# Kernel tuning notes

Hardware: AMD Instinct MI355X
Metric: run time of the kernel (lower is better)

The kernel has to match this reference:

```python
import jax, jax.numpy as jnp
import numpy as np
from jax import lax

B, SQ, SK, D, K = 4, 2048, 2048, 1024, 3


def setup_inputs() -> dict:
    key = jax.random.key(0)
    ks = jax.random.split(key, 16)
    s = 0.02
    return {
        "query_hidden": jax.random.normal(ks[0], (B, SQ, D), jnp.float32),
        "memory_hidden": jax.random.normal(ks[1], (B, SK, D), jnp.float32),
        "attention_mask": jax.random.randint(ks[2], (SQ, SK), 0, 2).astype(bool),
        # Linear projections (torch: y = x @ W.T + b)
        "q_w": jax.random.normal(ks[3], (D, D), jnp.float32) * s,
        "q_b": jnp.zeros((D,), jnp.float32),
        "k_w": jax.random.normal(ks[4], (D, D), jnp.float32) * s,
        "k_b": jnp.zeros((D,), jnp.float32),
        "v_w": jax.random.normal(ks[5], (D, D), jnp.float32) * s,
        "v_b": jnp.zeros((D,), jnp.float32),
        "o_w": jax.random.normal(ks[6], (D, D), jnp.float32) * s,
        "o_b": jnp.zeros((D,), jnp.float32),
        # ConvTransform1D: depthwise conv kernels [D,1,K], bias [D], scalar gate
        "q_kernel": jax.random.normal(ks[7], (D, 1, K), jnp.float32) * s,
        "q_cbias": jnp.zeros((D,), jnp.float32),
        "q_gate": jnp.zeros((), jnp.float32),
        "k_kernel": jax.random.normal(ks[8], (D, 1, K), jnp.float32) * s,
        "k_cbias": jnp.zeros((D,), jnp.float32),
        "k_gate": jnp.zeros((), jnp.float32),
        "v_kernel": jax.random.normal(ks[9], (D, 1, K), jnp.float32) * s,
        "v_cbias": jnp.zeros((D,), jnp.float32),
        "v_gate": jnp.zeros((), jnp.float32),
    }


def _conv_transform(x, kernel, cbias, gate):
    """Gated depthwise 1D conv along seq: x + tanh(gate) * dwconv(x). x: [B,S,D]."""
    xc = jnp.transpose(x, (0, 2, 1))  # [B,D,S]
    y = lax.conv_general_dilated(
        xc, kernel, window_strides=(1,), padding="SAME",
        dimension_numbers=("NCH", "OIH", "NCH"), feature_group_count=x.shape[-1])
    y = y + cbias[None, :, None]
    return x + jnp.tanh(gate) * jnp.transpose(y, (0, 2, 1))


def reference(query_hidden, memory_hidden, attention_mask,
              q_w, q_b, k_w, k_b, v_w, v_b, o_w, o_b,
              q_kernel, q_cbias, q_gate,
              k_kernel, k_cbias, k_gate,
              v_kernel, v_cbias, v_gate):
    d_model = query_hidden.shape[-1]
    q = _conv_transform(query_hidden @ q_w.T + q_b, q_kernel, q_cbias, q_gate)
    k = _conv_transform(memory_hidden @ k_w.T + k_b, k_kernel, k_cbias, k_gate)
    v = _conv_transform(memory_hidden @ v_w.T + v_b, v_kernel, v_cbias, v_gate)
    # [B,Sq,Sk]
    logits = jnp.einsum("bqd,bkd->bqk", q, k) / jnp.sqrt(jnp.float32(d_model))
    mask = attention_mask[None, :, :]  # broadcast like torch unsqueeze(0)
    logits = jnp.where(mask, logits, jnp.finfo(logits.dtype).min)
    attn = jax.nn.softmax(logits, axis=-1)
    out = jnp.einsum("bqk,bkd->bqd", attn, v) @ o_w.T + o_b
    return out
```

## Files before the change

### kernel.cpp

```cpp
#include <hip/hip_runtime.h>
#include <cstdint>
#include <cstddef>


#define GLOBAL_AS __attribute__((address_space(1)))
#define LDS_AS    __attribute__((address_space(3)))

typedef _Float16 h8 __attribute__((ext_vector_type(8)));
typedef float    f4_t __attribute__((ext_vector_type(4)));
typedef unsigned short us8 __attribute__((ext_vector_type(8)));

__device__ __forceinline__ float bf2f(unsigned short u) {
    union { unsigned int i; float f; } x; x.i = ((unsigned int)u) << 16; return x.f;
}
__device__ __forceinline__ float rd(const void* p, long i, int isBf) {
    return isBf ? bf2f(((const unsigned short*)p)[i]) : ((const float*)p)[i];
}

struct Probe16 { const unsigned short* p[16]; int n[16]; };

__global__ void k_probes(Probe16 a, const unsigned int* __restrict__ mask,
                         int* __restrict__ flags) {
    if (blockIdx.x < 16) {
        __shared__ int cnt;
        if (threadIdx.x == 0) cnt = 0;
        __syncthreads();
        const unsigned short* s = a.p[blockIdx.x];
        const int n = a.n[blockIdx.x];
        int bad = 0;
        for (int i = threadIdx.x; i < n; i += 256) {
            int e = (s[i] >> 7) & 0xFF;
            if (e >= 0x8F || (e > 0 && e <= 0x60)) bad++;
        }
        atomicAdd(&cnt, bad);
        __syncthreads();
        if (threadIdx.x == 0) flags[blockIdx.x] = (cnt * 4 > n) ? 0 : 1;
    } else {
        __shared__ int vi32, vf32, vbf, vf16;
        if (threadIdx.x == 0) { vi32 = vf32 = vbf = vf16 = 0; }
        __syncthreads();
        int bi32 = 0, bf32 = 0, bbf = 0, bf16c = 0;
        for (int i = threadIdx.x; i < 4096; i += 256) {
            unsigned int w = mask[i];
            if (!(w == 0u || w == 1u)) bi32++;
            if (!(w == 0u || w == 0x3F800000u)) bf32++;
            unsigned int h0 = w & 0xFFFFu, h1 = w >> 16;
            if (!((h0 == 0u || h0 == 0x3F80u) && (h1 == 0u || h1 == 0x3F80u))) bbf++;
            if (!((h0 == 0u || h0 == 0x3C00u) && (h1 == 0u || h1 == 0x3C00u))) bf16c++;
        }
        if (bi32) atomicAdd(&vi32, 1);
        if (bf32) atomicAdd(&vf32, 1);
        if (bbf)  atomicAdd(&vbf, 1);
        if (bf16c) atomicAdd(&vf16, 1);
        __syncthreads();
        if (threadIdx.x == 0) {
            int w;
            if (vi32 == 0) w = 4;
            else if (vf32 == 0) w = 4;
            else if (vbf == 0) w = 2;
            else if (vf16 == 0) w = 2;
            else w = 1;
            flags[16] = w;
        }
    }
}

__global__ void k_mask_bytes(const void* __restrict__ m, unsigned char* __restrict__ out,
                             long n, const int* __restrict__ widthFlag) {
    long i = ((long)blockIdx.x * 256 + threadIdx.x) * 4;
    if (i >= n) return;
    const int w = *widthFlag;
    unsigned int packed = 0;
    if (w == 4) {
        const unsigned int* p = (const unsigned int*)m;
#pragma unroll
        for (int u = 0; u < 4; ++u) packed |= (p[i + u] != 0u ? 1u : 0u) << (8 * u);
    } else if (w == 2) {
        const unsigned short* p = (const unsigned short*)m;
#pragma unroll
        for (int u = 0; u < 4; ++u) packed |= (p[i + u] != 0u ? 1u : 0u) << (8 * u);
    } else {
        const unsigned char* p = (const unsigned char*)m;
#pragma unroll
        for (int u = 0; u < 4; ++u) packed |= (p[i + u] != 0u ? 1u : 0u) << (8 * u);
    }
    *(unsigned int*)(out + i) = packed;
}

struct ConvSrc { const void* kern[3]; const void* cb[3]; const void* gate[3]; };
__global__ void k_conv_params(ConvSrc p, const int* __restrict__ flags,
                              _Float16* __restrict__ out, float* __restrict__ tg, int D) {
#pragma unroll
    for (int t = 0; t < 3; ++t) {
        const int kIs = flags[6 + t], cIs = flags[13 + t];
        for (int d = threadIdx.x; d < D; d += 256) {
#pragma unroll
            for (int j = 0; j < 3; ++j)
                out[t * 3 * D + j * D + d] = (_Float16)rd(p.kern[t], (long)d * 3 + j, kIs);
            out[9 * D + t * D + d] = (_Float16)rd(p.cb[t], d, cIs);
        }
    }
    if (threadIdx.x < 3) {
        const void* g = p.gate[threadIdx.x];
        float gv = rd(g, 0, ((const unsigned int*)g)[0] == 0u ? 1 : 0);
        tg[threadIdx.x] = tanhf(gv);
    }
}

__device__ __forceinline__ h8 cvt8(const void* src, size_t off8, int isBf) {
    h8 d;
    if (isBf) {
        us8 s = *(const us8*)((const unsigned short*)src + off8 * 8);
#pragma unroll
        for (int u = 0; u < 8; ++u) d[u] = (_Float16)bf2f(s[u]);
    } else {
        const float* f = (const float*)src + off8 * 8;
        f4_t a = *(const f4_t*)f;
        f4_t b = *(const f4_t*)(f + 4);
#pragma unroll
        for (int u = 0; u < 4; ++u) { d[u] = (_Float16)a[u]; d[4 + u] = (_Float16)b[u]; }
    }
    return d;
}

__global__ void k_h_to_f16(const void* __restrict__ s0, const void* __restrict__ s1,
                           _Float16* __restrict__ dst, int n8each,
                           const int* __restrict__ flags) {
    int i = blockIdx.x * blockDim.x + threadIdx.x;
    if (i >= 2 * n8each) return;
    int seg = i / n8each, off = i - seg * n8each;
    h8 d = cvt8(seg ? s1 : s0, off, flags[seg]);
    *(h8*)(dst + (size_t)i * 8) = d;
}

struct Ptr4 { const void* p[4]; };
__global__ void k_w_to_f16(Ptr4 srcs, _Float16* __restrict__ dst, int n8each,
                           const int* __restrict__ flags) {
    int i = blockIdx.x * blockDim.x + threadIdx.x;
    if (i >= 4 * n8each) return;
    int seg = i / n8each, off = i - seg * n8each;
    h8 d = cvt8(srcs.p[seg], off, flags[seg]);
    *(h8*)(dst + (size_t)i * 8) = d;
}

template <int MODE, int MTILE>
__global__ __launch_bounds__(256, 4) void k_gemm_nt(
    const _Float16* __restrict__ A, const _Float16* __restrict__ Bm,
    void* __restrict__ Cout,
    const void* __restrict__ bias, const int* __restrict__ biasFlag,
    const void* __restrict__ bias2, const int* __restrict__ biasFlag2,
    int N, int K, long sA, long sB, long sC,
    float scale, const unsigned char* __restrict__ mask8,
    int NT, int BZ) {

    constexpr int NI = (MTILE == 128) ? 4 : 2;
    constexpr int NCA = MTILE / 32;
    __shared__ __align__(16) _Float16 As[MTILE * 64];
    __shared__ __align__(16) _Float16 Bs[128 * 64];

    const long id = blockIdx.x;
    const int xcd = (int)(id & 7);
    const long local = id >> 3;
    const int col = (int)(local % NT);
    const long g = (local / NT) * 8 + xcd;
    const int bz = (int)(g % BZ);
    const int brow = (int)(g / BZ);

    const int tid  = threadIdx.x;
    const int wave = tid >> 6, lane = tid & 63;
    const int wm = (wave >> 1) * (MTILE / 2), wn = (wave & 1) * 64;
    const int lr = lane & 15, lq = lane >> 4;

    const _Float16* Ab = A + (long)bz * sA + (size_t)brow * MTILE * K;
    const _Float16* Bb = Bm + (long)bz * sB + (size_t)col * 128 * K;

    f4_t acc[NI][4] = {};

    const _Float16* gA[NCA];
    _Float16* lA[NCA];
#pragma unroll
    for (int j = 0; j < NCA; ++j) {
        int c = tid + j * 256;
        int r = c >> 3, s = ((c & 7) - r) & 7;
        gA[j] = Ab + (size_t)r * K + s * 8;
        lA[j] = As + c * 8;
    }
    const _Float16* gB[4];
    _Float16* lB[4];
#pragma unroll
    for (int j = 0; j < 4; ++j) {
        int c = tid + j * 256;
        int r = c >> 3, s = ((c & 7) - r) & 7;
        gB[j] = Bb + (size_t)r * K + s * 8;
        lB[j] = Bs + c * 8;
    }

    for (int kb = 0; kb < K; kb += 64) {
#pragma unroll
        for (int j = 0; j < NCA; ++j)
            __builtin_amdgcn_global_load_lds((void GLOBAL_AS*)(gA[j] + kb), (void LDS_AS*)lA[j], 16, 0, 0);
#pragma unroll
        for (int j = 0; j < 4; ++j)
            __builtin_amdgcn_global_load_lds((void GLOBAL_AS*)(gB[j] + kb), (void LDS_AS*)lB[j], 16, 0, 0);
        __syncthreads();

#pragma unroll
        for (int t = 0; t < 2; ++t) {
            const int fs = ((t * 4 + lq + lr) & 7) * 8;
            h8 af[NI], bfr[4];
#pragma unroll
            for (int i = 0; i < NI; ++i) af[i]  = *(const h8*)&As[(wm + i * 16 + lr) * 64 + fs];
#pragma unroll
            for (int j = 0; j < 4; ++j) bfr[j] = *(const h8*)&Bs[(wn + j * 16 + lr) * 64 + fs];
#pragma unroll
            for (int i = 0; i < NI; ++i)
#pragma unroll
                for (int j = 0; j < 4; ++j)
                    acc[i][j] = __builtin_amdgcn_mfma_f32_16x16x32_f16(af[i], bfr[j], acc[i][j], 0, 0, 0);
        }
        __syncthreads();
    }

    const long row0 = (long)brow * MTILE + wm + lq * 4;
    const long col0 = (long)col * 128 + wn + lr;

    if constexpr (MODE == 3) {
        _Float16* C = (_Float16*)Cout + (long)bz * sC;
#pragma unroll
        for (int i = 0; i < NI; ++i)
#pragma unroll
            for (int j = 0; j < 4; ++j)
#pragma unroll
                for (int r = 0; r < 4; ++r) {
                    long row = row0 + i * 16 + r;
                    long ccol = col0 + j * 16;
                    bool keep = mask8[row * (long)N + ccol] != 0;
                    float v = acc[i][j][r] * scale;
                    v = fminf(fmaxf(v, -60000.0f), 60000.0f);
                    C[row * (long)N + ccol] = (_Float16)(keep ? v : -60000.0f);
                }
    } else {
        float bv[4];
        if constexpr (MODE != 0) {
            const void* bp = bias; const int* bfp = biasFlag; long boff = 0;
            if (bias2 != nullptr && col * 128 >= (N >> 1)) {
                bp = bias2; bfp = biasFlag2; boff = (long)(N >> 1);
            }
            const int bIs = *bfp;
#pragma unroll
            for (int j = 0; j < 4; ++j) bv[j] = rd(bp, col0 + j * 16 - boff, bIs);
        } else {
#pragma unroll
            for (int j = 0; j < 4; ++j) bv[j] = 0.0f;
        }
        if constexpr (MODE == 2) {
            float* C = (float*)Cout + (long)bz * sC;
#pragma unroll
            for (int i = 0; i < NI; ++i)
#pragma unroll
                for (int j = 0; j < 4; ++j)
#pragma unroll
                    for (int r = 0; r < 4; ++r)
                        C[(row0 + i * 16 + r) * (long)N + col0 + j * 16] = acc[i][j][r] + bv[j];
        } else {
            _Float16* C = (_Float16*)Cout + (long)bz * sC;
#pragma unroll
            for (int i = 0; i < NI; ++i)
#pragma unroll
                for (int j = 0; j < 4; ++j)
#pragma unroll
                    for (int r = 0; r < 4; ++r) {
                        float v = acc[i][j][r] + bv[j];
                        v = fminf(fmaxf(v, -65000.0f), 65000.0f);
                        C[(row0 + i * 16 + r) * (long)N + col0 + j * 16] = (_Float16)v;
                    }
        }
    }
}

struct ConvP {
    const _Float16* x; int xs; _Float16* y;
    const _Float16* kp; const _Float16* cb; const float* tg;
};
__global__ void k_dwconv2(ConvP p0, ConvP p1, int S, int D) {
    const ConvP& p = blockIdx.z ? p1 : p0;
    int s = blockIdx.x, b = blockIdx.y;
    int d0 = threadIdx.x * 8;
    const size_t xb = ((size_t)b * S + s) * p.xs + d0;
    const size_t yb = ((size_t)b * S + s) * D + d0;
    h8 zero;
#pragma unroll
    for (int u = 0; u < 8; ++u) zero[u] = (_Float16)0.0f;
    h8 xc = *(const h8*)(p.x + xb);
    h8 xp = (s > 0)     ? *(const h8*)(p.x + xb - p.xs) : zero;
    h8 xn = (s < S - 1) ? *(const h8*)(p.x + xb + p.xs) : zero;
    h8 k0 = *(const h8*)(p.kp + 0 * D + d0);
    h8 k1 = *(const h8*)(p.kp + 1 * D + d0);
    h8 k2 = *(const h8*)(p.kp + 2 * D + d0);
    h8 cb = *(const h8*)(p.cb + d0);
    float tg = *p.tg;
    h8 o;
#pragma unroll
    for (int u = 0; u < 8; ++u) {
        float cv = (float)xp[u] * (float)k0[u] + (float)xc[u] * (float)k1[u] +
                   (float)xn[u] * (float)k2[u] + (float)cb[u];
        float v = (float)xc[u] + tg * cv;
        o[u] = (_Float16)fminf(fmaxf(v, -65000.0f), 65000.0f);
    }
    *(h8*)(p.y + yb) = o;
}

__global__ void k_dwconv_t(const _Float16* __restrict__ x, int xs,
                           _Float16* __restrict__ vt,
                           const _Float16* __restrict__ kp,
                           const _Float16* __restrict__ cbp,
                           const float* __restrict__ tgp,
                           int SK, int D) {
    __shared__ _Float16 T[64][65];
    int b = blockIdx.z;
    int s0 = blockIdx.x * 64, d0 = blockIdx.y * 64;
    int tid = threadIdx.x;
    float tg = *tgp;
    h8 zero;
#pragma unroll
    for (int u = 0; u < 8; ++u) zero[u] = (_Float16)0.0f;
#pragma unroll
    for (int it = 0; it < 2; ++it) {
        int idx = it * 256 + tid;
        int r = idx >> 3, c = (idx & 7) * 8;
        int s = s0 + r;
        const size_t xb = ((size_t)b * SK + s) * xs + d0 + c;
        h8 xc = *(const h8*)(x + xb);
        h8 xp = (s > 0)      ? *(const h8*)(x + xb - xs) : zero;
        h8 xn = (s < SK - 1) ? *(const h8*)(x + xb + xs) : zero;
        h8 k0 = *(const h8*)(kp + 0 * D + d0 + c);
        h8 k1 = *(const h8*)(kp + 1 * D + d0 + c);
        h8 k2 = *(const h8*)(kp + 2 * D + d0 + c);
        h8 cb = *(const h8*)(cbp + d0 + c);
#pragma unroll
        for (int u = 0; u < 8; ++u) {
            float cv = (float)xp[u] * (float)k0[u] + (float)xc[u] * (float)k1[u] +
                       (float)xn[u] * (float)k2[u] + (float)cb[u];
            float v = (float)xc[u] + tg * cv;
            T[r][c + u] = (_Float16)fminf(fmaxf(v, -65000.0f), 65000.0f);
        }
    }
    __syncthreads();
#pragma unroll
    for (int it = 0; it < 2; ++it) {
        int idx = it * 256 + tid;
        int dr = idx >> 3, c = (idx & 7) * 8;
        h8 o;
#pragma unroll
        for (int u = 0; u < 8; ++u) o[u] = T[c + u][dr];
        *(h8*)(vt + ((size_t)b * D + d0 + dr) * SK + s0 + c) = o;
    }
}

__global__ __launch_bounds__(256) void k_softmax(const _Float16* __restrict__ sc,
                                                 _Float16* __restrict__ pr, int SK) {
    const long row = blockIdx.x;
    const int tid = threadIdx.x, lane = tid & 63, wave = tid >> 6;
    h8 v = *(const h8*)(sc + row * (long)SK + tid * 8);
    float f[8]; float mx = -3.0e38f;
#pragma unroll
    for (int u = 0; u < 8; ++u) { f[u] = (float)v[u]; mx = fmaxf(mx, f[u]); }
#pragma unroll
    for (int o = 32; o > 0; o >>= 1) mx = fmaxf(mx, __shfl_xor(mx, o, 64));
    __shared__ float red[8];
    if (lane == 0) red[wave] = mx;
    __syncthreads();
    mx = fmaxf(fmaxf(red[0], red[1]), fmaxf(red[2], red[3]));
    float sum = 0.0f;
#pragma unroll
    for (int u = 0; u < 8; ++u) { f[u] = __expf(f[u] - mx); sum += f[u]; }
#pragma unroll
    for (int o = 32; o > 0; o >>= 1) sum += __shfl_xor(sum, o, 64);
    if (lane == 0) red[4 + wave] = sum;
    __syncthreads();
    sum = red[4] + red[5] + red[6] + red[7];
    float inv = 1.0f / sum;
    h8 o8;
#pragma unroll
    for (int u = 0; u < 8; ++u) o8[u] = (_Float16)(f[u] * inv);
    *(h8*)(pr + row * (long)SK + tid * 8) = o8;
}

extern "C" void kernel_launch(void* const* d_in, const int* in_sizes, int n_in,
                              void* d_out, int out_size, void* d_ws, size_t ws_size,
                              hipStream_t stream) {
    const int Bn = 4, SQ = 2048, SK = 2048, D = 1024;
    const size_t nQ = (size_t)Bn * SQ * D;
    const long   nM = (long)SQ * SK;

    const void* qh = d_in[0];
    const void* mh = d_in[1];
    const void* mask = d_in[2];
    const void* q_w = d_in[3];
    const void* q_b = d_in[4];
    const void* k_w = d_in[5];
    const void* k_b = d_in[6];
    const void* v_w = d_in[7];
    const void* v_b = d_in[8];
    const void* o_w = d_in[9];
    const void* o_b = d_in[10];
    const void* q_kern = d_in[11];
    const void* q_cb   = d_in[12];
    const void* q_g    = d_in[13];
    const void* k_kern = d_in[14];
    const void* k_cb   = d_in[15];
    const void* k_g    = d_in[16];
    const void* v_kern = d_in[17];
    const void* v_cb   = d_in[18];
    const void* v_g    = d_in[19];

    char* ws = (char*)d_ws;
    _Float16* scores   = (_Float16*)(ws + 0);
    _Float16* attn_out = (_Float16*)(ws + 0);
    _Float16* w16      = (_Float16*)(ws + 33554432);
    unsigned char* mask8 = (unsigned char*)(ws + 33554432);
    _Float16* par16    = (_Float16*)(ws + 37748736);
    float*    tgf      = (float*)(ws + 37748736 + 12 * 1024 * 2);
    _Float16* lin      = (_Float16*)(ws + 41943040);
    _Float16* lin_q    = lin;
    _Float16* lin_kv   = lin + nQ;
    _Float16* probs    = lin;
    _Float16* conv     = (_Float16*)(ws + 92274688);
    _Float16* qh16     = conv;
    _Float16* mh16     = conv + nQ;
    _Float16* vt       = (_Float16*)(ws + 125829120);
    int*      flags    = (int*)(ws + 142606336);

    Probe16 pa;
    const void* pp[16] = {qh, mh, q_w, k_w, v_w, o_w, q_kern, k_kern, v_kern,
                          q_b, k_b, v_b, o_b, q_cb, k_cb, v_cb};
    const int   pn[16] = {2048, 2048, 2048, 2048, 2048, 2048, 3072, 3072, 3072,
                          1024, 1024, 1024, 1024, 1024, 1024, 1024};
    for (int i = 0; i < 16; ++i) { pa.p[i] = (const unsigned short*)pp[i]; pa.n[i] = pn[i]; }
    k_probes<<<17, 256, 0, stream>>>(pa, (const unsigned int*)mask, flags);

    const int nH8 = (int)(nQ / 8);
    k_h_to_f16<<<(2 * nH8 + 255) / 256, 256, 0, stream>>>(qh, mh, qh16, nH8, flags + 0);
    const int nW8 = D * D / 8;
    Ptr4 wp; wp.p[0] = q_w; wp.p[1] = k_w; wp.p[2] = v_w; wp.p[3] = o_w;
    k_w_to_f16<<<(4 * nW8 + 255) / 256, 256, 0, stream>>>(wp, w16, nW8, flags + 2);

    k_gemm_nt<1, 64><<<dim3(1024), 256, 0, stream>>>(
        qh16, w16, lin_q, q_b, flags + 9, nullptr, nullptr,
        D, D, 0, 0, 0, 1.0f, nullptr, 8, 1);
    k_gemm_nt<1, 128><<<dim3(1024), 256, 0, stream>>>(
        mh16, w16 + (size_t)D * D, lin_kv, k_b, flags + 10, v_b, flags + 11,
        2 * D, D, 0, 0, 0, 1.0f, nullptr, 16, 1);

    k_mask_bytes<<<(int)(nM / 4 / 256), 256, 0, stream>>>(mask, mask8, nM, flags + 16);
    ConvSrc cs;
    cs.kern[0] = q_kern; cs.kern[1] = k_kern; cs.kern[2] = v_kern;
    cs.cb[0] = q_cb; cs.cb[1] = k_cb; cs.cb[2] = v_cb;
    cs.gate[0] = q_g; cs.gate[1] = k_g; cs.gate[2] = v_g;
    k_conv_params<<<1, 256, 0, stream>>>(cs, flags, par16, tgf, D);

    ConvP cq{lin_q, D, conv + 0 * nQ, par16 + 0 * 3 * D, par16 + 9 * D + 0 * D, tgf + 0};
    ConvP ck{lin_kv, 2 * D, conv + 1 * nQ, par16 + 1 * 3 * D, par16 + 9 * D + 1 * D, tgf + 1};
    k_dwconv2<<<dim3(SQ, Bn, 2), 128, 0, stream>>>(cq, ck, SQ, D);
    k_dwconv_t<<<dim3(SK / 64, D / 64, Bn), 256, 0, stream>>>(
        lin_kv + D, 2 * D, vt, par16 + 2 * 3 * D, par16 + 9 * D + 2 * D, tgf + 2, SK, D);

    k_gemm_nt<3, 128><<<dim3(1024), 256, 0, stream>>>(
        conv + 0 * nQ, conv + 1 * nQ, scores, nullptr, nullptr, nullptr, nullptr,
        SK, D, (long)SQ * D, (long)SK * D, (long)SQ * SK, 0.03125f, mask8, 16, 4);

    k_softmax<<<Bn * SQ, 256, 0, stream>>>(scores, probs, SK);

    k_gemm_nt<0, 64><<<dim3(1024), 256, 0, stream>>>(
        probs, vt, attn_out, nullptr, nullptr, nullptr, nullptr,
        D, SK, (long)SQ * SK, (long)D * SK, (long)SQ * D, 1.0f, nullptr, 8, 4);

    k_gemm_nt<2, 64><<<dim3(1024), 256, 0, stream>>>(
        attn_out, w16 + 3 * (size_t)D * D, d_out, o_b, flags + 12, nullptr, nullptr,
        D, D, 0, 0, 0, 1.0f, nullptr, 8, 1);

    (void)in_sizes; (void)n_in; (void)out_size; (void)ws_size;
}
```

Baseline: 409.4 us.

## Replace GEMMs with 8-wave 256x128 double-buffered pipelined kernel

Replaces the 4-wave, single-buffered NT GEMM with a 512-thread kernel that computes a 256x128 tile per block. It double-buffers A and B in LDS, issuing the next k-tile's global-to-LDS loads in two halves interleaved with the MFMA phases, and uses explicit vmcnt waits, barriers and setprio. The aim is to hide global load latency behind compute and raise per-block data reuse. The cost is 96KB of LDS per block, fewer blocks (256-512 instead of 1024), and correctness that depends on hand-placed waitcnt and barrier ordering.

Result: no change. 410.9 us (+0.4%).

```diff
diff --git a/kernel.cpp b/kernel.cpp
--- a/kernel.cpp
+++ b/kernel.cpp
@@ -143,8 +143,8 @@
     *(h8*)(dst + (size_t)i * 8) = d;
 }
 
-template <int MODE, int MTILE>
-__global__ __launch_bounds__(256, 4) void k_gemm_nt(
+template <int MODE>
+__global__ __launch_bounds__(512, 2) void k_gemm8(
     const _Float16* __restrict__ A, const _Float16* __restrict__ Bm,
     void* __restrict__ Cout,
     const void* __restrict__ bias, const int* __restrict__ biasFlag,
@@ -153,10 +153,8 @@
     float scale, const unsigned char* __restrict__ mask8,
     int NT, int BZ) {
 
-    constexpr int NI = (MTILE == 128) ? 4 : 2;
-    constexpr int NCA = MTILE / 32;
-    __shared__ __align__(16) _Float16 As[MTILE * 64];
-    __shared__ __align__(16) _Float16 Bs[128 * 64];
+    __shared__ __align__(16) _Float16 AS[2][256 * 64];
+    __shared__ __align__(16) _Float16 BS[2][128 * 64];
 
     const long id = blockIdx.x;
     const int xcd = (int)(id & 7);
@@ -168,66 +166,121 @@
 
     const int tid  = threadIdx.x;
     const int wave = tid >> 6, lane = tid & 63;
-    const int wm = (wave >> 1) * (MTILE / 2), wn = (wave & 1) * 64;
+    const int wr = wave >> 1, wc = wave & 1;
+    const int wmRow = wr * 64, wnRow = wc * 64;
     const int lr = lane & 15, lq = lane >> 4;
 
-    const _Float16* Ab = A + (long)bz * sA + (size_t)brow * MTILE * K;
+    const _Float16* Ab = A + (long)bz * sA + (size_t)brow * 256 * K;
     const _Float16* Bb = Bm + (long)bz * sB + (size_t)col * 128 * K;
 
-    f4_t acc[NI][4] = {};
-
-    const _Float16* gA[NCA];
-    _Float16* lA[NCA];
-#pragma unroll
-    for (int j = 0; j < NCA; ++j) {
-        int c = tid + j * 256;
+    f4_t acc[4][4] = {};
+
+    const _Float16* gA[4]; int lA[4];
+#pragma unroll
+    for (int j = 0; j < 4; ++j) {
+        int c = (tid & 255) + (j + 4 * (tid >> 8)) * 256;
         int r = c >> 3, s = ((c & 7) - r) & 7;
         gA[j] = Ab + (size_t)r * K + s * 8;
-        lA[j] = As + c * 8;
-    }
-    const _Float16* gB[4];
-    _Float16* lB[4];
-#pragma unroll
-    for (int j = 0; j < 4; ++j) {
-        int c = tid + j * 256;
+        lA[j] = c * 8;
+    }
+    const _Float16* gB[2]; int lB[2];
+#pragma unroll
+    for (int j = 0; j < 2; ++j) {
+        int c = tid + j * 512;
         int r = c >> 3, s = ((c & 7) - r) & 7;
         gB[j] = Bb + (size_t)r * K + s * 8;
-        lB[j] = Bs + c * 8;
-    }
-
-    for (int kb = 0; kb < K; kb += 64) {
-#pragma unroll
-        for (int j = 0; j < NCA; ++j)
-            __builtin_amdgcn_global_load_lds((void GLOBAL_AS*)(gA[j] + kb), (void LDS_AS*)lA[j], 16, 0, 0);
-#pragma unroll
-        for (int j = 0; j < 4; ++j)
-            __builtin_amdgcn_global_load_lds((void GLOBAL_AS*)(gB[j] + kb), (void LDS_AS*)lB[j], 16, 0, 0);
-        __syncthreads();
-
-#pragma unroll
-        for (int t = 0; t < 2; ++t) {
-            const int fs = ((t * 4 + lq + lr) & 7) * 8;
-            h8 af[NI], bfr[4];
-#pragma unroll
-            for (int i = 0; i < NI; ++i) af[i]  = *(const h8*)&As[(wm + i * 16 + lr) * 64 + fs];
-#pragma unroll
-            for (int j = 0; j < 4; ++j) bfr[j] = *(const h8*)&Bs[(wn + j * 16 + lr) * 64 + fs];
-#pragma unroll
-            for (int i = 0; i < NI; ++i)
-#pragma unroll
-                for (int j = 0; j < 4; ++j)
-                    acc[i][j] = __builtin_amdgcn_mfma_f32_16x16x32_f16(af[i], bfr[j], acc[i][j], 0, 0, 0);
-        }
-        __syncthreads();
-    }
-
-    const long row0 = (long)brow * MTILE + wm + lq * 4;
-    const long col0 = (long)col * 128 + wn + lr;
+        lB[j] = c * 8;
+    }
+
+    const int nkt = K >> 6;
+
+    __builtin_amdgcn_global_load_lds((void GLOBAL_AS*)gB[0], (void LDS_AS*)&BS[0][lB[0]], 16, 0, 0);
+    __builtin_amdgcn_global_load_lds((void GLOBAL_AS*)gB[1], (void LDS_AS*)&BS[0][lB[1]], 16, 0, 0);
+    __builtin_amdgcn_global_load_lds((void GLOBAL_AS*)gA[0], (void LDS_AS*)&AS[0][lA[0]], 16, 0, 0);
+    __builtin_amdgcn_global_load_lds((void GLOBAL_AS*)gA[2], (void LDS_AS*)&AS[0][lA[2]], 16, 0, 0);
+    __builtin_amdgcn_global_load_lds((void GLOBAL_AS*)gA[1], (void LDS_AS*)&AS[0][lA[1]], 16, 0, 0);
+    __builtin_amdgcn_global_load_lds((void GLOBAL_AS*)gA[3], (void LDS_AS*)&AS[0][lA[3]], 16, 0, 0);
+    asm volatile("s_waitcnt vmcnt(2)" ::: "memory");
+    __builtin_amdgcn_s_barrier();
+
+    int p = 0;
+    for (int t = 0; t < nkt; ++t) {
+        const _Float16* Ac = &AS[p][0];
+        const _Float16* Bc = &BS[p][0];
+        _Float16* An = &AS[p ^ 1][0];
+        _Float16* Bn = &BS[p ^ 1][0];
+        const bool pf = (t + 1) < nkt;
+        const long kb = (long)(t + 1) << 6;
+
+        h8 bfr[4][2], a0[2][2];
+#pragma unroll
+        for (int ks = 0; ks < 2; ++ks) {
+            const int fs = ((ks * 4 + lq + lr) & 7) * 8;
+#pragma unroll
+            for (int n = 0; n < 4; ++n)
+                bfr[n][ks] = *(const h8*)&Bc[(wnRow + n * 16 + lr) * 64 + fs];
+#pragma unroll
+            for (int i = 0; i < 2; ++i)
+                a0[i][ks] = *(const h8*)&Ac[(wmRow + i * 16 + lr) * 64 + fs];
+        }
+        if (pf) {
+            __builtin_amdgcn_global_load_lds((void GLOBAL_AS*)(gB[0] + kb), (void LDS_AS*)&Bn[lB[0]], 16, 0, 0);
+            __builtin_amdgcn_global_load_lds((void GLOBAL_AS*)(gB[1] + kb), (void LDS_AS*)&Bn[lB[1]], 16, 0, 0);
+            __builtin_amdgcn_global_load_lds((void GLOBAL_AS*)(gA[0] + kb), (void LDS_AS*)&An[lA[0]], 16, 0, 0);
+            __builtin_amdgcn_global_load_lds((void GLOBAL_AS*)(gA[2] + kb), (void LDS_AS*)&An[lA[2]], 16, 0, 0);
+        }
+        __builtin_amdgcn_s_barrier();
+        __builtin_amdgcn_s_setprio(1);
+#pragma unroll
+        for (int ks = 0; ks < 2; ++ks)
+#pragma unroll
+            for (int i = 0; i < 2; ++i)
+#pragma unroll
+                for (int n = 0; n < 4; ++n)
+                    acc[i][n] = __builtin_amdgcn_mfma_f32_16x16x32_f16(
+                        a0[i][ks], bfr[n][ks], acc[i][n], 0, 0, 0);
+        __builtin_amdgcn_s_setprio(0);
+        if (pf) asm volatile("s_waitcnt vmcnt(4)" ::: "memory");
+        else    asm volatile("s_waitcnt vmcnt(0)" ::: "memory");
+        __builtin_amdgcn_s_barrier();
+
+        h8 a1[2][2];
+#pragma unroll
+        for (int ks = 0; ks < 2; ++ks) {
+            const int fs = ((ks * 4 + lq + lr) & 7) * 8;
+#pragma unroll
+            for (int i = 0; i < 2; ++i)
+                a1[i][ks] = *(const h8*)&Ac[(wmRow + 32 + i * 16 + lr) * 64 + fs];
+        }
+        if (pf) {
+            __builtin_amdgcn_global_load_lds((void GLOBAL_AS*)(gA[1] + kb), (void LDS_AS*)&An[lA[1]], 16, 0, 0);
+            __builtin_amdgcn_global_load_lds((void GLOBAL_AS*)(gA[3] + kb), (void LDS_AS*)&An[lA[3]], 16, 0, 0);
+        }
+        __builtin_amdgcn_s_barrier();
+        __builtin_amdgcn_s_setprio(1);
+#pragma unroll
+        for (int ks = 0; ks < 2; ++ks)
+#pragma unroll
+            for (int i = 0; i < 2; ++i)
+#pragma unroll
+                for (int n = 0; n < 4; ++n)
+                    acc[2 + i][n] = __builtin_amdgcn_mfma_f32_16x16x32_f16(
+                        a1[i][ks], bfr[n][ks], acc[2 + i][n], 0, 0, 0);
+        __builtin_amdgcn_s_setprio(0);
+        if (pf) {
+            asm volatile("s_waitcnt vmcnt(2)" ::: "memory");
+            __builtin_amdgcn_s_barrier();
+        }
+        p ^= 1;
+    }
+
+    const long row0 = (long)brow * 256 + wmRow + lq * 4;
+    const long col0 = (long)col * 128 + wnRow + lr;
 
     if constexpr (MODE == 3) {
         _Float16* C = (_Float16*)Cout + (long)bz * sC;
 #pragma unroll
-        for (int i = 0; i < NI; ++i)
+        for (int i = 0; i < 4; ++i)
 #pragma unroll
             for (int j = 0; j < 4; ++j)
 #pragma unroll
@@ -256,7 +309,7 @@
         if constexpr (MODE == 2) {
             float* C = (float*)Cout + (long)bz * sC;
 #pragma unroll
-            for (int i = 0; i < NI; ++i)
+            for (int i = 0; i < 4; ++i)
 #pragma unroll
                 for (int j = 0; j < 4; ++j)
 #pragma unroll
@@ -265,7 +318,7 @@
         } else {
             _Float16* C = (_Float16*)Cout + (long)bz * sC;
 #pragma unroll
-            for (int i = 0; i < NI; ++i)
+            for (int i = 0; i < 4; ++i)
 #pragma unroll
                 for (int j = 0; j < 4; ++j)
 #pragma unroll
@@ -445,10 +498,10 @@
     Ptr4 wp; wp.p[0] = q_w; wp.p[1] = k_w; wp.p[2] = v_w; wp.p[3] = o_w;
     k_w_to_f16<<<(4 * nW8 + 255) / 256, 256, 0, stream>>>(wp, w16, nW8, flags + 2);
 
-    k_gemm_nt<1, 64><<<dim3(1024), 256, 0, stream>>>(
+    k_gemm8<1><<<dim3(256), 512, 0, stream>>>(
         qh16, w16, lin_q, q_b, flags + 9, nullptr, nullptr,
         D, D, 0, 0, 0, 1.0f, nullptr, 8, 1);
-    k_gemm_nt<1, 128><<<dim3(1024), 256, 0, stream>>>(
+    k_gemm8<1><<<dim3(512), 512, 0, stream>>>(
         mh16, w16 + (size_t)D * D, lin_kv, k_b, flags + 10, v_b, flags + 11,
         2 * D, D, 0, 0, 0, 1.0f, nullptr, 16, 1);
 
@@ -465,17 +518,17 @@
     k_dwconv_t<<<dim3(SK / 64, D / 64, Bn), 256, 0, stream>>>(
         lin_kv + D, 2 * D, vt, par16 + 2 * 3 * D, par16 + 9 * D + 2 * D, tgf + 2, SK, D);
 
-    k_gemm_nt<3, 128><<<dim3(1024), 256, 0, stream>>>(
+    k_gemm8<3><<<dim3(512), 512, 0, stream>>>(
         conv + 0 * nQ, conv + 1 * nQ, scores, nullptr, nullptr, nullptr, nullptr,
         SK, D, (long)SQ * D, (long)SK * D, (long)SQ * SK, 0.03125f, mask8, 16, 4);
 
     k_softmax<<<Bn * SQ, 256, 0, stream>>>(scores, probs, SK);
 
-    k_gemm_nt<0, 64><<<dim3(1024), 256, 0, stream>>>(
+    k_gemm8<0><<<dim3(256), 512, 0, stream>>>(
         probs, vt, attn_out, nullptr, nullptr, nullptr, nullptr,
         D, SK, (long)SQ * SK, (long)D * SK, (long)SQ * D, 1.0f, nullptr, 8, 4);
 
-    k_gemm_nt<2, 64><<<dim3(1024), 256, 0, stream>>>(
+    k_gemm8<2><<<dim3(256), 512, 0, stream>>>(
         attn_out, w16 + 3 * (size_t)D * D, d_out, o_b, flags + 12, nullptr, nullptr,
         D, D, 0, 0, 0, 1.0f, nullptr, 8, 1);
 
```

## Add 256x256-tile 8-wave GEMM with LDS-direct loads for KV and QK^T

Applied to the files above, without the earlier changes.

Adds a new k_gemm16 kernel with 256x256 output tiles, 512 threads (8 waves), double-buffered LDS fed by global_load_lds, and a four-phase interleaved schedule that prefetches quarter-tiles while running MFMAs at raised priority. The KV projection and the masked QK^T score GEMM now use it instead of the 128-wide k_gemm_nt. The aim is more data reuse per tile and better overlap of loads with compute. In exchange it uses large LDS and many registers, and only 256 blocks are launched. The old k_gemm_nt epilogue was also reshuffled so its MODE 3 masked path appears to be dropped from that kernel, though it is no longer called with MODE 3.

Result: no change. 411.1 us (+0.4%).

```diff
diff --git a/kernel.cpp b/kernel.cpp
--- a/kernel.cpp
+++ b/kernel.cpp
@@ -224,10 +224,231 @@
     const long row0 = (long)brow * MTILE + wm + lq * 4;
     const long col0 = (long)col * 128 + wn + lr;
 
+    {
+        float bv[4];
+        if constexpr (MODE != 0) {
+            const void* bp = bias; const int* bfp = biasFlag; long boff = 0;
+            if (bias2 != nullptr && col * 128 >= (N >> 1)) {
+                bp = bias2; bfp = biasFlag2; boff = (long)(N >> 1);
+            }
+            const int bIs = *bfp;
+#pragma unroll
+            for (int j = 0; j < 4; ++j) bv[j] = rd(bp, col0 + j * 16 - boff, bIs);
+        } else {
+#pragma unroll
+            for (int j = 0; j < 4; ++j) bv[j] = 0.0f;
+        }
+        if constexpr (MODE == 2) {
+            float* C = (float*)Cout + (long)bz * sC;
+#pragma unroll
+            for (int i = 0; i < NI; ++i)
+#pragma unroll
+                for (int j = 0; j < 4; ++j)
+#pragma unroll
+                    for (int r = 0; r < 4; ++r)
+                        C[(row0 + i * 16 + r) * (long)N + col0 + j * 16] = acc[i][j][r] + bv[j];
+        } else {
+            _Float16* C = (_Float16*)Cout + (long)bz * sC;
+#pragma unroll
+            for (int i = 0; i < NI; ++i)
+#pragma unroll
+                for (int j = 0; j < 4; ++j)
+#pragma unroll
+                    for (int r = 0; r < 4; ++r) {
+                        float v = acc[i][j][r] + bv[j];
+                        v = fminf(fmaxf(v, -65000.0f), 65000.0f);
+                        C[(row0 + i * 16 + r) * (long)N + col0 + j * 16] = (_Float16)v;
+                    }
+        }
+    }
+    (void)scale; (void)mask8;
+}
+
+template <int MODE>
+__global__ __launch_bounds__(512, 2) void k_gemm16(
+    const _Float16* __restrict__ A, const _Float16* __restrict__ Bm,
+    void* __restrict__ Cout,
+    const void* __restrict__ bias, const int* __restrict__ biasFlag,
+    const void* __restrict__ bias2, const int* __restrict__ biasFlag2,
+    int N, int K, long sA, long sB, long sC,
+    float scale, const unsigned char* __restrict__ mask8,
+    int NT, int BZ) {
+
+    __shared__ __align__(16) _Float16 AS[2][2][8192];
+    __shared__ __align__(16) _Float16 BS[2][2][8192];
+
+    const long id = blockIdx.x;
+    const int xcd = (int)(id & 7);
+    const long local = id >> 3;
+    const int col = (int)(local % NT);
+    const long g = (local / NT) * 8 + xcd;
+    const int bz = (int)(g % BZ);
+    const int brow = (int)(g / BZ);
+
+    const int tid  = threadIdx.x;
+    const int wave = tid >> 6, lane = tid & 63;
+    const int wr = wave >> 2, wc = wave & 3;
+    const int lr = lane & 15, lq = lane >> 4;
+
+    const _Float16* Ab = A + (long)bz * sA + (size_t)brow * 256 * K;
+    const _Float16* Bb = Bm + (long)bz * sB + (size_t)col * 256 * K;
+
+    f4_t acc[8][4] = {};
+
+    const _Float16* gAsrc[2][2];
+    const _Float16* gBsrc[2][2];
+    int lOff[2];
+#pragma unroll
+    for (int j = 0; j < 2; ++j) {
+        int c = tid + j * 512;
+        int rho = c >> 3, s = ((c & 7) - rho) & 7;
+        lOff[j] = c * 8;
+#pragma unroll
+        for (int gg = 0; gg < 2; ++gg) {
+            int ra = gg * 64 + (rho & 63) + (rho >> 6) * 128;
+            gAsrc[gg][j] = Ab + (size_t)ra * K + s * 8;
+            int rb = gg * 32 + (rho & 31) + (rho >> 5) * 64;
+            gBsrc[gg][j] = Bb + (size_t)rb * K + s * 8;
+        }
+    }
+
+#define STAGE_A(buf, gg, kb)                                                              \
+    do {                                                                                  \
+        __builtin_amdgcn_global_load_lds((void GLOBAL_AS*)(gAsrc[gg][0] + (kb)),          \
+                                         (void LDS_AS*)&AS[buf][gg][lOff[0]], 16, 0, 0);  \
+        __builtin_amdgcn_global_load_lds((void GLOBAL_AS*)(gAsrc[gg][1] + (kb)),          \
+                                         (void LDS_AS*)&AS[buf][gg][lOff[1]], 16, 0, 0);  \
+    } while (0)
+#define STAGE_B(buf, gg, kb)                                                              \
+    do {                                                                                  \
+        __builtin_amdgcn_global_load_lds((void GLOBAL_AS*)(gBsrc[gg][0] + (kb)),          \
+                                         (void LDS_AS*)&BS[buf][gg][lOff[0]], 16, 0, 0);  \
+        __builtin_amdgcn_global_load_lds((void GLOBAL_AS*)(gBsrc[gg][1] + (kb)),          \
+                                         (void LDS_AS*)&BS[buf][gg][lOff[1]], 16, 0, 0);  \
+    } while (0)
+
+    const int nkt = K >> 6;
+
+    STAGE_A(0, 0, 0);
+    STAGE_B(0, 0, 0);
+    STAGE_B(0, 1, 0);
+    STAGE_A(0, 1, 0);
+    asm volatile("s_waitcnt vmcnt(4)" ::: "memory");
+    __builtin_amdgcn_s_barrier();
+
+    int cur = 0;
+    for (int t = 0; t < nkt; ++t) {
+        const bool pf = (t + 1) < nkt;
+        const long kb = (long)(t + 1) << 6;
+        const int nx = cur ^ 1;
+        h8 a0[4][2], a1[4][2], b0[2][2], b1[2][2];
+
+#pragma unroll
+        for (int ks = 0; ks < 2; ++ks) {
+#pragma unroll
+            for (int m = 0; m < 4; ++m) {
+                int rho = wr * 64 + m * 16 + lr;
+                a0[m][ks] = *(const h8*)&AS[cur][0][rho * 64 + ((ks * 4 + lq + rho) & 7) * 8];
+            }
+#pragma unroll
+            for (int n = 0; n < 2; ++n) {
+                int rho = wc * 32 + n * 16 + lr;
+                b0[n][ks] = *(const h8*)&BS[cur][0][rho * 64 + ((ks * 4 + lq + rho) & 7) * 8];
+            }
+        }
+        if (pf) STAGE_A(nx, 0, kb);
+        __builtin_amdgcn_s_barrier();
+        __builtin_amdgcn_s_setprio(1);
+#pragma unroll
+        for (int ks = 0; ks < 2; ++ks)
+#pragma unroll
+            for (int m = 0; m < 4; ++m)
+#pragma unroll
+                for (int n = 0; n < 2; ++n)
+                    acc[m][n] = __builtin_amdgcn_mfma_f32_16x16x32_f16(
+                        a0[m][ks], b0[n][ks], acc[m][n], 0, 0, 0);
+        __builtin_amdgcn_s_setprio(0);
+        if (pf) asm volatile("s_waitcnt vmcnt(4)" ::: "memory");
+        else    asm volatile("s_waitcnt vmcnt(2)" ::: "memory");
+        __builtin_amdgcn_s_barrier();
+
+#pragma unroll
+        for (int ks = 0; ks < 2; ++ks)
+#pragma unroll
+            for (int n = 0; n < 2; ++n) {
+                int rho = wc * 32 + n * 16 + lr;
+                b1[n][ks] = *(const h8*)&BS[cur][1][rho * 64 + ((ks * 4 + lq + rho) & 7) * 8];
+            }
+        if (pf) STAGE_B(nx, 0, kb);
+        __builtin_amdgcn_s_barrier();
+        __builtin_amdgcn_s_setprio(1);
+#pragma unroll
+        for (int ks = 0; ks < 2; ++ks)
+#pragma unroll
+            for (int m = 0; m < 4; ++m)
+#pragma unroll
+                for (int n = 0; n < 2; ++n)
+                    acc[m][2 + n] = __builtin_amdgcn_mfma_f32_16x16x32_f16(
+                        a0[m][ks], b1[n][ks], acc[m][2 + n], 0, 0, 0);
+        __builtin_amdgcn_s_setprio(0);
+        if (pf) asm volatile("s_waitcnt vmcnt(4)" ::: "memory");
+        else    asm volatile("s_waitcnt vmcnt(0)" ::: "memory");
+        __builtin_amdgcn_s_barrier();
+
+#pragma unroll
+        for (int ks = 0; ks < 2; ++ks)
+#pragma unroll
+            for (int m = 0; m < 4; ++m) {
+                int rho = wr * 64 + m * 16 + lr;
+                a1[m][ks] = *(const h8*)&AS[cur][1][rho * 64 + ((ks * 4 + lq + rho) & 7) * 8];
+            }
+        if (pf) STAGE_B(nx, 1, kb);
+        __builtin_amdgcn_s_barrier();
+        __builtin_amdgcn_s_setprio(1);
+#pragma unroll
+        for (int ks = 0; ks < 2; ++ks)
+#pragma unroll
+            for (int m = 0; m < 4; ++m)
+#pragma unroll
+                for (int n = 0; n < 2; ++n)
+                    acc[4 + m][2 + n] = __builtin_amdgcn_mfma_f32_16x16x32_f16(
+                        a1[m][ks], b1[n][ks], acc[4 + m][2 + n], 0, 0, 0);
+        __builtin_amdgcn_s_setprio(0);
+        __builtin_amdgcn_s_barrier();
+
+#pragma unroll
+        for (int ks = 0; ks < 2; ++ks)
+#pragma unroll
+            for (int n = 0; n < 2; ++n) {
+                int rho = wc * 32 + n * 16 + lr;
+                b0[n][ks] = *(const h8*)&BS[cur][0][rho * 64 + ((ks * 4 + lq + rho) & 7) * 8];
+            }
+        if (pf) STAGE_A(nx, 1, kb);
+        __builtin_amdgcn_s_barrier();
+        __builtin_amdgcn_s_setprio(1);
+#pragma unroll
+        for (int ks = 0; ks < 2; ++ks)
+#pragma unroll
+            for (int m = 0; m < 4; ++m)
+#pragma unroll
+                for (int n = 0; n < 2; ++n)
+                    acc[4 + m][n] = __builtin_amdgcn_mfma_f32_16x16x32_f16(
+                        a1[m][ks], b0[n][ks], acc[4 + m][n], 0, 0, 0);
+        __builtin_amdgcn_s_setprio(0);
+        if (pf) asm volatile("s_waitcnt vmcnt(4)" ::: "memory");
+        __builtin_amdgcn_s_barrier();
+        cur = nx;
+    }
+#undef STAGE_A
+#undef STAGE_B
+
+    const long row0 = (long)brow * 256 + wr * 128 + lq * 4;
+    const long col0 = (long)col * 256 + wc * 64 + lr;
+
     if constexpr (MODE == 3) {
         _Float16* C = (_Float16*)Cout + (long)bz * sC;
 #pragma unroll
-        for (int i = 0; i < NI; ++i)
+        for (int i = 0; i < 8; ++i)
 #pragma unroll
             for (int j = 0; j < 4; ++j)
 #pragma unroll
@@ -241,40 +462,26 @@
                 }
     } else {
         float bv[4];
-        if constexpr (MODE != 0) {
+        {
             const void* bp = bias; const int* bfp = biasFlag; long boff = 0;
-            if (bias2 != nullptr && col * 128 >= (N >> 1)) {
+            if (bias2 != nullptr && col * 256 >= (N >> 1)) {
                 bp = bias2; bfp = biasFlag2; boff = (long)(N >> 1);
             }
             const int bIs = *bfp;
 #pragma unroll
             for (int j = 0; j < 4; ++j) bv[j] = rd(bp, col0 + j * 16 - boff, bIs);
-        } else {
-#pragma unroll
-            for (int j = 0; j < 4; ++j) bv[j] = 0.0f;
-        }
-        if constexpr (MODE == 2) {
-            float* C = (float*)Cout + (long)bz * sC;
-#pragma unroll
-            for (int i = 0; i < NI; ++i)
-#pragma unroll
-                for (int j = 0; j < 4; ++j)
-#pragma unroll
-                    for (int r = 0; r < 4; ++r)
-                        C[(row0 + i * 16 + r) * (long)N + col0 + j * 16] = acc[i][j][r] + bv[j];
-        } else {
-            _Float16* C = (_Float16*)Cout + (long)bz * sC;
-#pragma unroll
-            for (int i = 0; i < NI; ++i)
-#pragma unroll
-                for (int j = 0; j < 4; ++j)
-#pragma unroll
-                    for (int r = 0; r < 4; ++r) {
-                        float v = acc[i][j][r] + bv[j];
-                        v = fminf(fmaxf(v, -65000.0f), 65000.0f);
-                        C[(row0 + i * 16 + r) * (long)N + col0 + j * 16] = (_Float16)v;
-                    }
-        }
+        }
+        _Float16* C = (_Float16*)Cout + (long)bz * sC;
+#pragma unroll
+        for (int i = 0; i < 8; ++i)
+#pragma unroll
+            for (int j = 0; j < 4; ++j)
+#pragma unroll
+                for (int r = 0; r < 4; ++r) {
+                    float v = acc[i][j][r] + bv[j];
+                    v = fminf(fmaxf(v, -65000.0f), 65000.0f);
+                    C[(row0 + i * 16 + r) * (long)N + col0 + j * 16] = (_Float16)v;
+                }
     }
 }
 
@@ -448,9 +655,9 @@
     k_gemm_nt<1, 64><<<dim3(1024), 256, 0, stream>>>(
         qh16, w16, lin_q, q_b, flags + 9, nullptr, nullptr,
         D, D, 0, 0, 0, 1.0f, nullptr, 8, 1);
-    k_gemm_nt<1, 128><<<dim3(1024), 256, 0, stream>>>(
+    k_gemm16<1><<<dim3(256), 512, 0, stream>>>(
         mh16, w16 + (size_t)D * D, lin_kv, k_b, flags + 10, v_b, flags + 11,
-        2 * D, D, 0, 0, 0, 1.0f, nullptr, 16, 1);
+        2 * D, D, 0, 0, 0, 1.0f, nullptr, 8, 1);
 
     k_mask_bytes<<<(int)(nM / 4 / 256), 256, 0, stream>>>(mask, mask8, nM, flags + 16);
     ConvSrc cs;
@@ -465,9 +672,9 @@
     k_dwconv_t<<<dim3(SK / 64, D / 64, Bn), 256, 0, stream>>>(
         lin_kv + D, 2 * D, vt, par16 + 2 * 3 * D, par16 + 9 * D + 2 * D, tgf + 2, SK, D);
 
-    k_gemm_nt<3, 128><<<dim3(1024), 256, 0, stream>>>(
+    k_gemm16<3><<<dim3(256), 512, 0, stream>>>(
         conv + 0 * nQ, conv + 1 * nQ, scores, nullptr, nullptr, nullptr, nullptr,
-        SK, D, (long)SQ * D, (long)SK * D, (long)SQ * SK, 0.03125f, mask8, 16, 4);
+        SK, D, (long)SQ * D, (long)SK * D, (long)SQ * SK, 0.03125f, mask8, 8, 4);
 
     k_softmax<<<Bn * SQ, 256, 0, stream>>>(scores, probs, SK);
 
```
